# Performance work log

Hardware: AMD Instinct MI355X
Metric: run time of the kernel (lower is better)

The kernel has to match this reference:

```python
import jax, jax.numpy as jnp
import numpy as np

S, B, D, E, F = 2048, 2, 1024, 8, 4096


def setup_inputs() -> dict:
    key = jax.random.key(0)
    ks = jax.random.split(key, 6)
    x = jax.random.normal(ks[0], (S, B, D), dtype=jnp.float32)
    w_switch = jax.random.normal(ks[1], (D, E), dtype=jnp.float32) / np.sqrt(D)
    b_switch = jnp.zeros((E,), dtype=jnp.float32)
    w1 = jax.random.normal(ks[2], (E, D, F), dtype=jnp.float32) / np.sqrt(D)
    b1 = jnp.zeros((E, F), dtype=jnp.float32)
    w2 = jax.random.normal(ks[3], (E, F, D), dtype=jnp.float32) / np.sqrt(F)
    b2 = jnp.zeros((E, D), dtype=jnp.float32)
    return {"x": x, "w_switch": w_switch, "b_switch": b_switch,
            "w1": w1, "b1": b1, "w2": w2, "b2": b2}


def reference(x, w_switch, b_switch, w1, b1, w2, b2):
    # x: [S, B, D] -> tokens [N, D]
    s, b, d = x.shape
    n_experts = w1.shape[0]
    xf = x.reshape(-1, d)                                    # [N, D]
    route_prob = jax.nn.softmax(xf @ w_switch + b_switch, axis=-1)  # [N, E]
    route_prob_max = jnp.max(route_prob, axis=-1)            # [N]
    routes = jnp.argmax(route_prob, axis=-1)                 # [N] int
    # is_scale_prob=True: scale token by its routing probability before FFN
    xs = xf * route_prob_max[:, None]                        # [N, D]
    # Per-expert FFN evaluated densely (drop_tokens=False => every token kept),
    # then each token selects its routed expert's output.
    h = jax.nn.relu(jnp.einsum('nd,edf->enf', xs, w1) + b1[:, None, :])  # [E, N, F]
    y = jnp.einsum('enf,efd->end', h, w2) + b2[:, None, :]               # [E, N, D]
    n = xf.shape[0]
    out = y[routes, jnp.arange(n)]                           # [N, D]
    counts = jnp.zeros((n_experts,), dtype=jnp.float32).at[routes].add(1.0)
    n_dropped = jnp.zeros((), dtype=jnp.int32)               # drop_tokens=False
    return out.reshape(s, b, d), counts, route_prob.sum(0), n_dropped
```

## Files before the change

kernel.cpp:

```cpp
#include <hip/hip_runtime.h>
#include <hip/hip_bf16.h>

#define NTOK 4096
#define DDIM 1024
#define NEXP 8
#define FDIM 4096
#define MAXTILES 40

typedef __attribute__((ext_vector_type(4))) float f32x4;
typedef __attribute__((ext_vector_type(8))) short bf16x8;
typedef __attribute__((ext_vector_type(8))) unsigned short u16x8;

#define GLDS(g, l) __builtin_amdgcn_global_load_lds( \
    (const __attribute__((address_space(1))) unsigned int*)(g), \
    (__attribute__((address_space(3))) unsigned int*)(l), 16, 0, 0)

__global__ __launch_bounds__(256) void route_kernel(
    const float* __restrict__ x,
    const float* __restrict__ w_switch,
    const float* __restrict__ b_switch,
    __hip_bfloat16* __restrict__ xs,
    int* __restrict__ amax_arr,
    float* __restrict__ partial)
{
    const int tid = threadIdx.x;
    const int wave = tid >> 6, lane = tid & 63;
    __shared__ float pr[4][16];

    float wacc[16];
#pragma unroll
    for (int j = 0; j < 16; j++) wacc[j] = 0.0f;

    for (int i = 0; i < 4; i++) {
        const int n = blockIdx.x * 16 + wave * 4 + i;
        const float4* xr = (const float4*)(x + (size_t)n * DDIM);
        float4 xv[4];
#pragma unroll
        for (int j = 0; j < 4; j++) xv[j] = xr[lane + j * 64];

        float acc[NEXP];
#pragma unroll
        for (int e = 0; e < NEXP; e++) acc[e] = 0.0f;
#pragma unroll
        for (int j = 0; j < 4; j++) {
            const int dbase = (lane + j * 64) * 4;
#pragma unroll
            for (int c = 0; c < 4; c++) {
                const float4* wr = (const float4*)(w_switch + (size_t)(dbase + c) * NEXP);
                float4 w0 = wr[0], w1 = wr[1];
                float xvc = ((const float*)&xv[j])[c];
                acc[0] += xvc * w0.x; acc[1] += xvc * w0.y;
                acc[2] += xvc * w0.z; acc[3] += xvc * w0.w;
                acc[4] += xvc * w1.x; acc[5] += xvc * w1.y;
                acc[6] += xvc * w1.z; acc[7] += xvc * w1.w;
            }
        }
#pragma unroll
        for (int e = 0; e < NEXP; e++) {
            float v = acc[e];
#pragma unroll
            for (int off = 32; off > 0; off >>= 1) v += __shfl_xor(v, off, 64);
            acc[e] = v;
        }
        float mx = -1e30f;
#pragma unroll
        for (int e = 0; e < NEXP; e++) {
            acc[e] += b_switch[e];
            mx = fmaxf(mx, acc[e]);
        }
        float sum = 0.0f;
#pragma unroll
        for (int e = 0; e < NEXP; e++) { acc[e] = __expf(acc[e] - mx); sum += acc[e]; }
        float inv = 1.0f / sum;
        float pmax = -1.0f; int amax = 0;
#pragma unroll
        for (int e = 0; e < NEXP; e++) {
            float p = acc[e] * inv;
            acc[e] = p;
            if (p > pmax) { pmax = p; amax = e; }
        }
#pragma unroll
        for (int e = 0; e < NEXP; e++) {
            wacc[e] += acc[e];
            wacc[8 + e] += (amax == e) ? 1.0f : 0.0f;
        }
        if (lane == 0) amax_arr[n] = amax;
#pragma unroll
        for (int j = 0; j < 4; j++) {
            ushort4 pk;
            __hip_bfloat16* pp = (__hip_bfloat16*)&pk;
            pp[0] = __float2bfloat16(xv[j].x * pmax);
            pp[1] = __float2bfloat16(xv[j].y * pmax);
            pp[2] = __float2bfloat16(xv[j].z * pmax);
            pp[3] = __float2bfloat16(xv[j].w * pmax);
            *(ushort4*)(xs + (size_t)n * DDIM + (lane + j * 64) * 4) = pk;
        }
    }
    if (lane == 0) {
#pragma unroll
        for (int j = 0; j < 16; j++) pr[wave][j] = wacc[j];
    }
    __syncthreads();
    if (tid < 16)
        partial[blockIdx.x * 16 + tid] = pr[0][tid] + pr[1][tid] + pr[2][tid] + pr[3][tid];
}

__global__ __launch_bounds__(1024) void bucket_kernel(
    const int* __restrict__ amax_arr, int* __restrict__ bucket, int* __restrict__ ecnt)
{
    const int e = blockIdx.x;
    __shared__ int ctr;
    if (threadIdx.x == 0) ctr = 0;
    __syncthreads();
    const int lane = threadIdx.x & 63;
    for (int c = 0; c < NTOK; c += 1024) {
        int t = c + threadIdx.x;
        bool my = (amax_arr[t] == e);
        unsigned long long mask = __ballot(my);
        int cnt = __popcll(mask);
        int base = 0;
        if (lane == 0 && cnt) base = atomicAdd(&ctr, cnt);
        base = __shfl(base, 0, 64);
        if (my) {
            int rank = __popcll(mask & ((1ull << lane) - 1ull));
            bucket[e * NTOK + base + rank] = t;
        }
    }
    __syncthreads();
    if (threadIdx.x == 0) ecnt[e] = ctr;
}

__global__ __launch_bounds__(256) void finalize_table_kernel(
    const float* __restrict__ partial, const int* __restrict__ ecnt,
    float* __restrict__ out_tail, int* __restrict__ table)
{
    __shared__ float red[16][16];
    const int j = threadIdx.x & 15, g = threadIdx.x >> 4;
    float s = 0.0f;
    for (int k = 0; k < 16; k++) s += partial[(size_t)(g + k * 16) * 16 + j];
    red[g][j] = s;
    __syncthreads();
    if (threadIdx.x < 16) {
        float t = 0.0f;
        for (int k = 0; k < 16; k++) t += red[k][threadIdx.x];
        int dst = (threadIdx.x < 8) ? (8 + threadIdx.x) : (threadIdx.x - 8);
        out_tail[dst] = t;
    }
    if (threadIdx.x == 16) out_tail[16] = 0.0f;
    if (threadIdx.x == 0) {
        int idx = 0;
        for (int e = 0; e < NEXP; e++) {
            int cnt = ecnt[e];
            for (int m0 = 0; m0 < cnt; m0 += 128) table[idx++] = (e << 16) | m0;
        }
        for (; idx < MAXTILES; idx++) table[idx] = -1;
    }
}

__global__ __launch_bounds__(256) void init_out_kernel(
    const float* __restrict__ b2, const int* __restrict__ amax_arr,
    float* __restrict__ out)
{
    const int t = blockIdx.x;
    const int e = amax_arr[t];
    const float4* br = (const float4*)(b2 + (size_t)e * DDIM);
    ((float4*)(out + (size_t)t * DDIM))[threadIdx.x] = br[threadIdx.x];
}

template <int R, int C>
__global__ __launch_bounds__(256) void transpose_kernel(
    const float* __restrict__ in, __hip_bfloat16* __restrict__ outp)
{
    const int e = blockIdx.z;
    const int r0 = blockIdx.y * 64, c0 = blockIdx.x * 64;
    __shared__ __hip_bfloat16 t[64 * 65];
    const int tid = threadIdx.x;
    const int ri = tid >> 4, c4 = (tid & 15) * 4;
    const float* src = in + ((size_t)e * R + r0) * C + c0;
#pragma unroll
    for (int rr = 0; rr < 4; rr++) {
        int r = ri + rr * 16;
        float4 v = *(const float4*)(src + (size_t)r * C + c4);
        t[r * 65 + c4 + 0] = __float2bfloat16(v.x);
        t[r * 65 + c4 + 1] = __float2bfloat16(v.y);
        t[r * 65 + c4 + 2] = __float2bfloat16(v.z);
        t[r * 65 + c4 + 3] = __float2bfloat16(v.w);
    }
    __syncthreads();
    const int co = tid >> 2, m = tid & 3;
    u16x8 v0, v1;
#pragma unroll
    for (int idx = 0; idx < 8; idx++)
        ((unsigned short*)&v0)[idx] = *(const unsigned short*)&t[(m * 16 + idx) * 65 + co];
#pragma unroll
    for (int idx = 0; idx < 8; idx++)
        ((unsigned short*)&v1)[idx] = *(const unsigned short*)&t[(m * 16 + idx + 8) * 65 + co];
    __hip_bfloat16* dst = outp + ((size_t)e * C + c0 + co) * R + r0 + m * 16;
    *(u16x8*)(dst) = v0;
    *(u16x8*)(dst + 8) = v1;
}

template <int MODE, int K, int NN, int KS>
__device__ __forceinline__ void gemm_body(
    const __hip_bfloat16* __restrict__ A,
    const __hip_bfloat16* __restrict__ Bt,
    const float* __restrict__ bias,
    const int* __restrict__ bucket,
    const int* __restrict__ ecnt,
    const int* __restrict__ table,
    void* __restrict__ Out)
{
    const int entry = table[blockIdx.y];
    if (entry < 0) return;
    const int e = entry >> 16;
    const int m0 = entry & 0xffff;
    const int cnt = ecnt[e];
    const int n0 = blockIdx.x * 128;
    const int kbase = (K / KS) * blockIdx.z;

    __shared__ __align__(16) __hip_bfloat16 Asm[2][128 * 32];
    __shared__ __align__(16) __hip_bfloat16 Bsm[2][128 * 32];
    __shared__ int toks[128];

    const int tid = threadIdx.x;
    if (tid < 128) {
        int r = m0 + tid;
        toks[tid] = bucket[e * NTOK + (r < cnt ? r : cnt - 1)];
    }
    __syncthreads();

    const int wave = tid >> 6, lane = tid & 63;
    const int r = lane & 15, kq = lane >> 4;
    const int g0 = 2 * wave;

    const __hip_bfloat16* pA0 = A + (size_t)toks[g0 * 16 + r] * K + kbase + kq * 8;
    const __hip_bfloat16* pA1 = A + (size_t)toks[(g0 + 1) * 16 + r] * K + kbase + kq * 8;
    const __hip_bfloat16* pB0 = Bt + ((size_t)e * NN + n0 + g0 * 16 + r) * K + kbase + kq * 8;
    const __hip_bfloat16* pB1 = Bt + ((size_t)e * NN + n0 + (g0 + 1) * 16 + r) * K + kbase + kq * 8;
    char* lA = (char*)Asm + g0 * 1024;
    char* lB = (char*)Bsm + g0 * 1024;

    const int wm = wave & 1, wn = wave >> 1;
    f32x4 acc[4][4];
#pragma unroll
    for (int t = 0; t < 4; t++)
#pragma unroll
        for (int u = 0; u < 4; u++) acc[t][u] = (f32x4){0.f, 0.f, 0.f, 0.f};

    constexpr int NSTEP = (K / KS) / 32;

    GLDS(pA0, lA); GLDS(pA1, lA + 1024);
    GLDS(pB0, lB); GLDS(pB1, lB + 1024);
    pA0 += 32; pA1 += 32; pB0 += 32; pB1 += 32;
    asm volatile("s_waitcnt vmcnt(0)" ::: "memory");
    __builtin_amdgcn_s_barrier();

    int cur = 0;
    for (int t = 0; t < NSTEP; ++t) {
        if (t + 1 < NSTEP) {
            const int so = (cur ^ 1) * 8192;
            GLDS(pA0, lA + so); GLDS(pA1, lA + so + 1024);
            GLDS(pB0, lB + so); GLDS(pB1, lB + so + 1024);
            pA0 += 32; pA1 += 32; pB0 += 32; pB1 += 32;
        }
        const char* Ab = (const char*)Asm + cur * 8192;
        const char* Bb = (const char*)Bsm + cur * 8192;
        bf16x8 a[4], b[4];
#pragma unroll
        for (int t4 = 0; t4 < 4; t4++)
            a[t4] = *(const bf16x8*)(Ab + (wm * 4 + t4) * 1024 + lane * 16);
#pragma unroll
        for (int u = 0; u < 4; u++)
            b[u] = *(const bf16x8*)(Bb + (wn * 4 + u) * 1024 + lane * 16);
#pragma unroll
        for (int t4 = 0; t4 < 4; t4++)
#pragma unroll
            for (int u = 0; u < 4; u++)
                acc[t4][u] = __builtin_amdgcn_mfma_f32_16x16x32_bf16(a[t4], b[u], acc[t4][u], 0, 0, 0);
        if (t + 1 < NSTEP) {
            asm volatile("s_waitcnt vmcnt(0)" ::: "memory");
            __builtin_amdgcn_s_barrier();
        }
        cur ^= 1;
    }

    const int quad = lane >> 4, l15 = lane & 15;
    float bv[4];
#pragma unroll
    for (int u = 0; u < 4; u++)
        bv[u] = (MODE == 0) ? bias[(size_t)e * NN + n0 + wn * 64 + u * 16 + l15] : 0.0f;
#pragma unroll
    for (int t = 0; t < 4; t++) {
#pragma unroll
        for (int rr = 0; rr < 4; rr++) {
            int row = wm * 64 + t * 16 + quad * 4 + rr;
            if (m0 + row < cnt) {
                int tok = toks[row];
#pragma unroll
                for (int u = 0; u < 4; u++) {
                    int col = n0 + wn * 64 + u * 16 + l15;
                    float v = acc[t][u][rr] + bv[u];
                    if (MODE == 0) {
                        v = fmaxf(v, 0.0f);
                        ((__hip_bfloat16*)Out)[(size_t)tok * NN + col] = __float2bfloat16(v);
                    } else {
                        unsafeAtomicAdd(&((float*)Out)[(size_t)tok * NN + col], v);
                    }
                }
            }
        }
    }
}

__global__ __launch_bounds__(256) void gemm_ffn1(
    const __hip_bfloat16* __restrict__ A, const __hip_bfloat16* __restrict__ Bt,
    const float* __restrict__ bias, const int* __restrict__ bucket,
    const int* __restrict__ ecnt, const int* __restrict__ table, void* __restrict__ Out)
{
    gemm_body<0, DDIM, FDIM, 1>(A, Bt, bias, bucket, ecnt, table, Out);
}

__global__ __launch_bounds__(256) void gemm_ffn2(
    const __hip_bfloat16* __restrict__ A, const __hip_bfloat16* __restrict__ Bt,
    const float* __restrict__ bias, const int* __restrict__ bucket,
    const int* __restrict__ ecnt, const int* __restrict__ table, void* __restrict__ Out)
{
    gemm_body<1, FDIM, DDIM, 2>(A, Bt, bias, bucket, ecnt, table, Out);
}

extern "C" void kernel_launch(void* const* d_in, const int* in_sizes, int n_in,
                              void* d_out, int out_size, void* d_ws, size_t ws_size,
                              hipStream_t stream) {
    const float* x        = (const float*)d_in[0];
    const float* w_switch = (const float*)d_in[1];
    const float* b_switch = (const float*)d_in[2];
    const float* w1       = (const float*)d_in[3];
    const float* b1       = (const float*)d_in[4];
    const float* w2       = (const float*)d_in[5];
    const float* b2       = (const float*)d_in[6];

    float* out = (float*)d_out;
    float* out_tail = out + (size_t)NTOK * DDIM;

    char* ws = (char*)d_ws;
    __hip_bfloat16* xs = (__hip_bfloat16*)(ws);
    __hip_bfloat16* h  = (__hip_bfloat16*)(ws + 8388608ull);
    __hip_bfloat16* wt = (__hip_bfloat16*)(ws + 41943040ull);
    int* bucket        = (int*)(ws + 109051904ull);
    int* amax_arr      = (int*)(ws + 109182976ull);
    float* partial     = (float*)(ws + 109199360ull);
    int* ecnt          = (int*)(ws + 109215744ull);
    int* table         = (int*)(ws + 109215776ull);

    hipLaunchKernelGGL(route_kernel, dim3(256), dim3(256), 0, stream,
                       x, w_switch, b_switch, xs, amax_arr, partial);
    hipLaunchKernelGGL(bucket_kernel, dim3(NEXP), dim3(1024), 0, stream,
                       amax_arr, bucket, ecnt);
    hipLaunchKernelGGL(finalize_table_kernel, dim3(1), dim3(256), 0, stream,
                       partial, ecnt, out_tail, table);
    hipLaunchKernelGGL(init_out_kernel, dim3(NTOK), dim3(256), 0, stream,
                       b2, amax_arr, out);

    hipLaunchKernelGGL((transpose_kernel<DDIM, FDIM>), dim3(FDIM / 64, DDIM / 64, NEXP),
                       dim3(256), 0, stream, w1, wt);
    hipLaunchKernelGGL(gemm_ffn1, dim3(FDIM / 128, MAXTILES), dim3(256), 0, stream,
                       xs, wt, b1, bucket, ecnt, table, (void*)h);

    hipLaunchKernelGGL((transpose_kernel<FDIM, DDIM>), dim3(DDIM / 64, FDIM / 64, NEXP),
                       dim3(256), 0, stream, w2, wt);
    hipLaunchKernelGGL(gemm_ffn2, dim3(DDIM / 128, MAXTILES, 2), dim3(256), 0, stream,
                       h, wt, b2, bucket, ecnt, table, (void*)out);
}
```

Before: 536.3 us.

## Triple-buffer GEMM LDS pipeline and raise FFN2 split-K to four

The GEMM main loop moves from a double-buffered LDS staging scheme to a triple-buffered one. Loads are issued two K-steps ahead, and the loop waits with vmcnt(4) so one stage of global-to-LDS loads stays in flight during the MFMAs. The second FFN GEMM also splits K four ways instead of two, giving it more blocks. This adds 16KB more LDS per block, which may lower occupancy, and doubles the atomic or partial-output accumulation traffic for FFN2.

```diff
diff --git a/kernel.cpp b/kernel.cpp
--- a/kernel.cpp
+++ b/kernel.cpp
@@ -218,8 +218,8 @@
     const int n0 = blockIdx.x * 128;
     const int kbase = (K / KS) * blockIdx.z;
 
-    __shared__ __align__(16) __hip_bfloat16 Asm[2][128 * 32];
-    __shared__ __align__(16) __hip_bfloat16 Bsm[2][128 * 32];
+    __shared__ __align__(16) __hip_bfloat16 Asm[3][128 * 32];
+    __shared__ __align__(16) __hip_bfloat16 Bsm[3][128 * 32];
     __shared__ int toks[128];
 
     const int tid = threadIdx.x;
@@ -237,8 +237,6 @@
     const __hip_bfloat16* pA1 = A + (size_t)toks[(g0 + 1) * 16 + r] * K + kbase + kq * 8;
     const __hip_bfloat16* pB0 = Bt + ((size_t)e * NN + n0 + g0 * 16 + r) * K + kbase + kq * 8;
     const __hip_bfloat16* pB1 = Bt + ((size_t)e * NN + n0 + (g0 + 1) * 16 + r) * K + kbase + kq * 8;
-    char* lA = (char*)Asm + g0 * 1024;
-    char* lB = (char*)Bsm + g0 * 1024;
 
     const int wm = wave & 1, wn = wave >> 1;
     f32x4 acc[4][4];
@@ -248,23 +246,27 @@
         for (int u = 0; u < 4; u++) acc[t][u] = (f32x4){0.f, 0.f, 0.f, 0.f};
 
     constexpr int NSTEP = (K / KS) / 32;
-
-    GLDS(pA0, lA); GLDS(pA1, lA + 1024);
-    GLDS(pB0, lB); GLDS(pB1, lB + 1024);
-    pA0 += 32; pA1 += 32; pB0 += 32; pB1 += 32;
-    asm volatile("s_waitcnt vmcnt(0)" ::: "memory");
+    static_assert(NSTEP >= 2, "pipeline needs >=2 K-steps");
+
+    auto stage = [&](int b) {
+        char* la = (char*)Asm + b * 8192 + g0 * 1024;
+        char* lb = (char*)Bsm + b * 8192 + g0 * 1024;
+        GLDS(pA0, la); GLDS(pA1, la + 1024);
+        GLDS(pB0, lb); GLDS(pB1, lb + 1024);
+        pA0 += 32; pA1 += 32; pB0 += 32; pB1 += 32;
+    };
+
+    stage(0);
+    stage(1);
+    asm volatile("s_waitcnt vmcnt(4)" ::: "memory");
     __builtin_amdgcn_s_barrier();
 
-    int cur = 0;
     for (int t = 0; t < NSTEP; ++t) {
-        if (t + 1 < NSTEP) {
-            const int so = (cur ^ 1) * 8192;
-            GLDS(pA0, lA + so); GLDS(pA1, lA + so + 1024);
-            GLDS(pB0, lB + so); GLDS(pB1, lB + so + 1024);
-            pA0 += 32; pA1 += 32; pB0 += 32; pB1 += 32;
-        }
-        const char* Ab = (const char*)Asm + cur * 8192;
-        const char* Bb = (const char*)Bsm + cur * 8192;
+        const int cb = t % 3;
+        if (t + 2 < NSTEP) stage((t + 2) % 3);
+
+        const char* Ab = (const char*)Asm + cb * 8192;
+        const char* Bb = (const char*)Bsm + cb * 8192;
         bf16x8 a[4], b[4];
 #pragma unroll
         for (int t4 = 0; t4 < 4; t4++)
@@ -277,11 +279,14 @@
 #pragma unroll
             for (int u = 0; u < 4; u++)
                 acc[t4][u] = __builtin_amdgcn_mfma_f32_16x16x32_bf16(a[t4], b[u], acc[t4][u], 0, 0, 0);
-        if (t + 1 < NSTEP) {
+
+        if (t + 2 < NSTEP) {
+            asm volatile("s_waitcnt vmcnt(4)" ::: "memory");
+            __builtin_amdgcn_s_barrier();
+        } else if (t + 1 < NSTEP) {
             asm volatile("s_waitcnt vmcnt(0)" ::: "memory");
             __builtin_amdgcn_s_barrier();
         }
-        cur ^= 1;
     }
 
     const int quad = lane >> 4, l15 = lane & 15;
@@ -325,7 +330,7 @@
     const float* __restrict__ bias, const int* __restrict__ bucket,
     const int* __restrict__ ecnt, const int* __restrict__ table, void* __restrict__ Out)
 {
-    gemm_body<1, FDIM, DDIM, 2>(A, Bt, bias, bucket, ecnt, table, Out);
+    gemm_body<1, FDIM, DDIM, 4>(A, Bt, bias, bucket, ecnt, table, Out);
 }
 
 extern "C" void kernel_launch(void* const* d_in, const int* in_sizes, int n_in,
@@ -368,6 +373,6 @@
 
     hipLaunchKernelGGL((transpose_kernel<FDIM, DDIM>), dim3(DDIM / 64, FDIM / 64, NEXP),
                        dim3(256), 0, stream, w2, wt);
-    hipLaunchKernelGGL(gemm_ffn2, dim3(DDIM / 128, MAXTILES, 2), dim3(256), 0, stream,
+    hipLaunchKernelGGL(gemm_ffn2, dim3(DDIM / 128, MAXTILES, 4), dim3(256), 0, stream,
                        h, wt, b2, bucket, ecnt, table, (void*)out);
 }
```

Result: slower. 556.1 us (+3.7%).
